# Kernel tuning notes

Hardware: AMD Instinct MI355X
Metric: run time of the kernel (lower is better)

Reference implementation:

```python
import jax, jax.numpy as jnp
from jax import lax
import numpy as np

BETA, TAU, NUM_ITER = 0.33, 1.0, 5
DN = ('NCDHW', 'OIDHW', 'NCDHW')


def _base_kernels():
    # 3x3x3 neighborhood-counting kernels from the torch module
    K_N6 = np.zeros((3, 3, 3), np.float32)
    for c in [(1, 1, 0), (1, 1, 2), (1, 0, 1), (1, 2, 1), (0, 1, 1), (2, 1, 1)]:
        K_N6[c] = 1.0
    K_N26 = np.ones((3, 3, 3), np.float32); K_N26[1, 1, 1] = 0.0
    K_N18 = K_N26.copy()
    for c in [(0, 0, 0), (0, 0, 2), (0, 2, 0), (0, 2, 2), (2, 0, 0), (2, 0, 2), (2, 2, 0), (2, 2, 2)]:
        K_N18[c] = 0.0
    K_B26 = np.zeros((3, 3, 3), np.float32)
    K_B26[0, 0, 0] = 1.0
    for c in [(0, 0, 1), (0, 1, 0), (0, 1, 1), (1, 0, 0), (1, 0, 1), (1, 1, 0)]:
        K_B26[c] = -1.0
    K_A6 = np.zeros((3, 3, 3), np.float32)
    K_A6[0, 1, 1] = -1.0
    for c in [(0, 0, 1), (0, 1, 0), (0, 1, 2), (0, 2, 1)]:
        K_A6[c] = 1.0
    return K_N6, K_N26, K_N18, K_B26, K_A6


def _stacked_weight():
    # Fuse all 17 simple-check convolutions into one conv over a 3-channel input
    # channel 0: img, channel 1: 1-img, channel 2: 2*img-1
    K_N6, K_N26, K_N18, K_B26, K_A6 = _base_kernels()
    b26 = [K_B26] + [np.flip(K_B26, ax) for ax in [(0,), (1,), (2,), (0, 1), (0, 2), (1, 2), (0, 1, 2)]]
    fA = np.flip(K_A6, 0)
    a6 = [K_A6, np.rot90(K_A6, axes=(0, 1)), np.rot90(K_A6, axes=(0, 2)),
          fA, np.rot90(fA, axes=(0, 1)), np.rot90(fA, axes=(0, 2))]
    rows = []
    def put(k, ch):
        w = np.zeros((3, 3, 3, 3), np.float32)
        w[ch] = k
        rows.append(w)
    put(K_N6, 1)   # counts bg 6-neighbors (applied to 1-img)
    put(K_N26, 0)  # counts fg 26-neighbors
    put(K_N18, 0)  # counts fg 18-neighbors
    for k in b26:
        put(k, 2)  # 8 B26-cell detectors on 2*img-1
    for k in a6:
        put(k, 2)  # 6 A6-cell detectors on 2*img-1
    return jnp.asarray(np.stack(rows)), jnp.asarray(K_N26).reshape(1, 1, 3, 3, 3)


W_SIMPLE, W_N26 = _stacked_weight()


def _clip01(x):  # F.hardtanh(x, 0, 1)
    return jnp.clip(x, 0.0, 1.0)


def _endpoint_check(img):
    p = jnp.pad(img, ((0, 0), (0, 0), (1, 1), (1, 1), (1, 1)))
    n26 = lax.conv_general_dilated(p, W_N26, (1, 1, 1), 'VALID', dimension_numbers=DN)
    return _clip01(2.0 - n26)  # endpoint iff <=1 fg 26-neighbor


def _simple_check(img):
    p = jnp.pad(img, ((0, 0), (0, 0), (1, 1), (1, 1), (1, 1)))
    x3 = jnp.concatenate([p, 1.0 - p, 2.0 * p - 1.0], axis=1)
    f = lax.conv_general_dilated(x3, W_SIMPLE, (2, 2, 2), 'VALID', dimension_numbers=DN)
    n6, n26, n18 = f[:, 0:1], f[:, 1:2], f[:, 2:3]
    num_b26 = jax.nn.relu(f[:, 3:11] - 6.0).sum(axis=1, keepdims=True)
    num_a6 = jax.nn.relu(f[:, 11:17] - 4.0).sum(axis=1, keepdims=True)
    cond1 = _clip01(n6) * _clip01(2.0 - n6)                              # exactly one bg 6-neighbor
    cond2 = _clip01(n26) * _clip01(2.0 - n26)                            # exactly one fg 26-neighbor
    cond3 = _clip01(n18) * _clip01(2.0 - n18) * _clip01(1.0 - num_b26)   # one 18-neighbor, no B26 cell
    cond4 = _clip01(n6 - 1.0) * _clip01(1.0 - num_a6) * _clip01(1.0 - num_b26)  # >=2 bg 6-nb, no A6/B26 cell
    return _clip01(cond1 + cond2 + cond3 + cond4)


def _forward(img):
    # _prepare_input: zero-pad each spatial dim by 1
    img = jnp.pad(img, ((0, 0), (0, 0), (1, 1), (1, 1), (1, 1)))
    # _stochastic_discretization (reparametrization + straight-through)
    alpha = (img + 1e-8) / (1.0 - img + 1e-8)
    u = jax.random.uniform(jax.random.key(42), img.shape, img.dtype, 1e-8, 1.0 - 1e-8)
    noise = jnp.log(u) - jnp.log1p(-u)
    soft = jax.nn.sigmoid((jnp.log(alpha) + noise * BETA) / TAU)
    img = lax.stop_gradient((soft > 0.5).astype(soft.dtype) - soft) + soft
    offsets = [(0, 0, 0), (1, 0, 0), (0, 1, 0), (1, 1, 0), (0, 0, 1), (1, 0, 1), (0, 1, 1), (1, 1, 1)]
    for _ in range(NUM_ITER):
        is_end = _endpoint_check(img)
        for xo, yo, zo in offsets:
            is_simple = _simple_check(img[:, :, xo:, yo:, zo:])
            sl = (slice(None), slice(None), slice(xo, None, 2), slice(yo, None, 2), slice(zo, None, 2))
            del_cand = is_simple * (1.0 - is_end[sl])
            img = img.at[sl].set(jnp.minimum(img[sl], 1.0 - del_cand))
    # _prepare_output: strip padding
    return img[:, :, 1:-1, 1:-1, 1:-1]


def setup_inputs():
    key = jax.random.key(0)
    img = jax.random.uniform(key, (2, 1, 160, 160, 160), jnp.float32)  # probabilities in [0,1)
    return {"img": img}


def reference(img):
    return _forward(img)
```

## Files before the change

kernel.cpp:

```cpp
#include <hip/hip_runtime.h>
#include <stdint.h>

#pragma clang fp contract(off)

#define PDIM 162
#define NW   (2*PDIM*PDIM*3)
#define NWH  (NW/2)
#define OD   160

#define PZ 97
#define LADDR(lz,ly) ((lz)*PZ + (ly)*3)

__device__ __forceinline__ uint32_t rotl32(uint32_t x, uint32_t r) {
  return (x << r) | (x >> (32u - r));
}

__device__ __forceinline__ uint32_t threefry_bits(uint32_t idx) {
  const uint32_t ks0 = 0u, ks1 = 42u, ks2 = 0x1BD11BDAu ^ 0u ^ 42u;
  uint32_t x0 = 0u + ks0;
  uint32_t x1 = idx + ks1;
#define TFR(r) { x0 += x1; x1 = rotl32(x1, (r)); x1 ^= x0; }
  TFR(13u) TFR(15u) TFR(26u) TFR(6u)
  x0 += ks1; x1 += ks2 + 1u;
  TFR(17u) TFR(29u) TFR(16u) TFR(24u)
  x0 += ks2; x1 += ks0 + 2u;
  TFR(13u) TFR(15u) TFR(26u) TFR(6u)
  x0 += ks0; x1 += ks1 + 3u;
  TFR(17u) TFR(29u) TFR(16u) TFR(24u)
  x0 += ks1; x1 += ks2 + 4u;
  TFR(13u) TFR(15u) TFR(26u) TFR(6u)
  x0 += ks2; x1 += ks0 + 5u;
#undef TFR
  return x0 ^ x1;
}

__device__ __forceinline__ float xla_logf(float xin) {
  uint32_t bits = __float_as_uint(xin);
  float e = (float)((int)(bits >> 23) - 126);
  float x = __uint_as_float((bits & 0x007fffffu) | 0x3f000000u);
  const float SQRTHF = 0.707106781186547524f;
  bool lt = (x < SQRTHF);
  float tmp = lt ? x : 0.0f;
  e = e - (lt ? 1.0f : 0.0f);
  x = x - 1.0f;
  x = x + tmp;
  float z = x * x;
  float y = 7.0376836292e-2f;
  y = fmaf(y, x, -1.1514610310e-1f);
  y = fmaf(y, x,  1.1676998740e-1f);
  y = fmaf(y, x, -1.2420140846e-1f);
  y = fmaf(y, x,  1.4249322787e-1f);
  y = fmaf(y, x, -1.6668057665e-1f);
  y = fmaf(y, x,  2.0000714765e-1f);
  y = fmaf(y, x, -2.4999993993e-1f);
  y = fmaf(y, x,  3.3333331174e-1f);
  y = y * x;
  y = y * z;
  y = fmaf(e, -2.12194440e-4f, y);
  y = fmaf(-0.5f, z, y);
  x = x + y;
  x = fmaf(e, 0.693359375f, x);
  return x;
}

__device__ __forceinline__ float xla_log1pf(float x) {
  float for_large = xla_logf(x + 1.0f);
  float for_small = fmaf(-0.5f, x, 1.0f) * x;
  return (fabsf(x) < 1e-4f) ? for_small : for_large;
}

__device__ __forceinline__ bool bin_pred(const float* __restrict__ in, uint32_t w,
                                         uint32_t lane) {
  uint32_t row = w / 3u, wx = w - row * 3u;
  uint32_t n  = row / (uint32_t)(PDIM * PDIM);
  uint32_t rr = row - n * (uint32_t)(PDIM * PDIM);
  uint32_t z  = rr / (uint32_t)PDIM;
  uint32_t y  = rr - z * (uint32_t)PDIM;
  uint32_t x  = wx * 64u + lane;
  if ((z - 1u) >= 160u || (y - 1u) >= 160u || (x - 1u) >= 160u) return false;
  float v = in[((n * 160u + (z - 1u)) * 160u + (y - 1u)) * 160u + (x - 1u)];
  uint32_t i = row * 162u + x;
  uint32_t b = threefry_bits(i);
  float f  = __uint_as_float((b >> 9) | 0x3f800000u) - 1.0f;
  float uu = fmaxf(1e-8f, f + 1e-8f);
  float h  = (v + 1e-8f) / ((1.0f - v) + 1e-8f);
  const float T = 1.1920928955078125e-7f;

  const float LN2 = 0.6931471805599453f;
  float la_f = __builtin_amdgcn_logf(h) * LN2;
  float nz_f = (__builtin_amdgcn_logf(uu) - __builtin_amdgcn_logf(1.0f - uu)) * LN2;
  float zs_f = fmaf(nz_f, 0.33f, la_f);
  if (fabsf(zs_f - T) > 3.0e-4f) return zs_f > T;

  float la = xla_logf(h);
  float noise = xla_logf(uu) - xla_log1pf(-uu);
  float zs = la + noise * 0.33f;
  return zs > T;
}

__global__ __launch_bounds__(256) void k_binarize(const float* __restrict__ in,
                                                  uint64_t* __restrict__ bits) {
  uint32_t t = blockIdx.x * 256u + threadIdx.x;
  uint32_t w0 = t >> 6, lane = t & 63u;
  if (w0 >= (uint32_t)NWH) return;
  uint32_t w1 = w0 + (uint32_t)NWH;
  bool p0 = bin_pred(in, w0, lane);
  bool p1 = bin_pred(in, w1, lane);
  uint64_t m0 = __ballot(p0);
  uint64_t m1 = __ballot(p1);
  if (lane == 0) { bits[w0] = m0; bits[w1] = m1; }
}

#define NB(dz,dy,dx) ((dx)==-1 ? Lb[(dz)+1][(dy)+1] : ((dx)==1 ? Rb[(dz)+1][(dy)+1] : Vv[(dz)+1][(dy)+1]))

#define GATHER_W(SRC, lz, ly, w) \
  _Pragma("unroll") \
  for (int dz = 0; dz < 3; ++dz) \
    _Pragma("unroll") \
    for (int dy = 0; dy < 3; ++dy) { \
      int rb = LADDR((lz) + dz - 1, (ly) + dy - 1); \
      uint64_t r0 = SRC[rb], r1 = SRC[rb + 1], r2 = SRC[rb + 2]; \
      uint64_t b = ((w) == 0) ? r0 : (((w) == 1) ? r1 : r2); \
      uint64_t a = ((w) == 0) ? 0ull : (((w) == 1) ? r0 : r1); \
      uint64_t d = ((w) == 0) ? r1 : (((w) == 1) ? r2 : 0ull); \
      Vv[dz][dy] = b; \
      Lb[dz][dy] = (b << 1) | (a >> 63); \
      Rb[dz][dy] = (b >> 1) | (d << 63); \
    }

struct OG { uint64_t o, g; };
__device__ __forceinline__ OG og_leaf2(uint64_t a, uint64_t b) {
  OG r; r.o = a | b; r.g = a & b; return r;
}
__device__ __forceinline__ OG og_comb(OG a, OG b) {
  OG r; r.g = a.g | b.g | (a.o & b.o); r.o = a.o | b.o; return r;
}

#define OG_BUILD_18_C(og18, ogc) \
  OG a0 = og_leaf2(NB(-1,0,0), NB(1,0,0)); \
  OG a1 = og_leaf2(NB(0,-1,0), NB(0,1,0)); \
  OG a2 = og_leaf2(NB(0,0,-1), NB(0,0,1)); \
  OG e0 = og_leaf2(NB(-1,-1,0), NB(-1,1,0)); \
  OG e1 = og_leaf2(NB(-1,0,-1), NB(-1,0,1)); \
  OG e2 = og_leaf2(NB(1,-1,0),  NB(1,1,0)); \
  OG e3 = og_leaf2(NB(1,0,-1),  NB(1,0,1)); \
  OG e4 = og_leaf2(NB(0,-1,-1), NB(0,-1,1)); \
  OG e5 = og_leaf2(NB(0,1,-1),  NB(0,1,1)); \
  OG t0 = og_comb(a0, a1); \
  OG t1 = og_comb(a2, e0); \
  OG t2 = og_comb(e1, e2); \
  OG t3 = og_comb(e3, e4); \
  OG og18 = og_comb(og_comb(og_comb(t0, t1), og_comb(t2, t3)), e5); \
  OG c0 = og_leaf2(NB(-1,-1,-1), NB(-1,-1,1)); \
  OG c1 = og_leaf2(NB(-1,1,-1),  NB(-1,1,1)); \
  OG c2 = og_leaf2(NB(1,-1,-1),  NB(1,-1,1)); \
  OG c3 = og_leaf2(NB(1,1,-1),   NB(1,1,1)); \
  OG ogc = og_comb(og_comb(c0, c1), og_comb(c2, c3));

__global__ __launch_bounds__(1024) void k_iter(const uint64_t* __restrict__ bin,
                                               uint64_t* __restrict__ bout,
                                               float4* __restrict__ outf,
                                               int zero_pads) {
  __shared__ uint64_t Bt[32 * PZ];
  __shared__ uint64_t Ge[32 * PZ];
  const int tid = threadIdx.x;
  const int bid = blockIdx.x;
  const int n  = bid / 100;
  const int rm = bid - n * 100;
  const int tz = rm / 10, ty = rm - tz * 10;
  const int gz0 = 1 + 16 * tz, gy0 = 1 + 16 * ty;

  if (zero_pads && bid == 0) {
    for (int j = tid; j < 1288; j += 1024) {
      int nn, z, y;
      if (j < 648) { nn = j / 324; int r = j - nn * 324;
                     z = (r >= 162) ? 161 : 0; y = (r >= 162) ? r - 162 : r; }
      else { int j2 = j - 648; nn = j2 / 320; int r = j2 - nn * 320;
             y = (r >= 160) ? 161 : 0; z = 1 + ((r >= 160) ? r - 160 : r); }
      uint64_t* p = bout + (((nn * 162 + z) * 162) + y) * 3;
      p[0] = 0; p[1] = 0; p[2] = 0;
    }
  }

  for (int ti = tid; ti < 32 * 32 * 3; ti += 1024) {
    int w = ti % 3, r = ti / 3, ly = r % 32, lz = r / 32;
    int z = gz0 - 8 + lz, y = gy0 - 8 + ly;
    uint64_t v = 0;
    if ((unsigned)z < 162u && (unsigned)y < 162u)
      v = bin[((n * 162 + z) * 162 + y) * 3 + w];
    Bt[LADDR(lz, ly) + w] = v;
  }
  __syncthreads();

  for (int ti = tid; ti < 30 * 30 * 3; ti += 1024) {
    int w = ti % 3, r = ti / 3, iy = r % 30, iz = r / 30;
    int lz = 1 + iz, ly = 1 + iy;
    int base = LADDR(lz, ly) + w;
    uint64_t res = 0;
    if (Bt[base] != 0ull) {
      uint64_t Vv[3][3], Lb[3][3], Rb[3][3];
      GATHER_W(Bt, lz, ly, w)
      OG_BUILD_18_C(og18, ogc)
      res = og_comb(og18, ogc).g;
    }
    Ge[base] = res;
  }
  __syncthreads();

  const int PLZ[8] = {1,0,1,0,1,0,1,0};
  const int PLY[8] = {1,1,0,0,1,1,0,0};
#pragma unroll
  for (int k = 0; k < 8; ++k) {
    const int h = 7 - k, cnt1 = 8 + h;
    const uint64_t xmask = (k < 4) ? 0x5555555555555555ull : 0xAAAAAAAAAAAAAAAAull;
    const int s0 = 8 - h;
    const int slz = s0 + ((s0 ^ PLZ[k]) & 1);
    const int sly = s0 + ((s0 ^ PLY[k]) & 1);
    for (int ti = tid; ti < cnt1 * cnt1 * 3; ti += 1024) {
      int w = ti % 3, r = ti / 3, iy = r % cnt1, iz = r / cnt1;
      int lz = slz + 2 * iz, ly = sly + 2 * iy;
      int base = LADDR(lz, ly) + w;
      uint64_t center = Bt[base];
      uint64_t act = center & xmask & Ge[base];
      if (act == 0ull) continue;
      uint64_t Vv[3][3], Lb[3][3], Rb[3][3];
      GATHER_W(Bt, lz, ly, w)

      OG_BUILD_18_C(og18, ogc)
      OG og26 = og_comb(og18, ogc);
      uint64_t e18 = og18.o & ~og18.g;
      uint64_t e26 = og26.o & ~og26.g;

      uint64_t m0f = ~NB(-1,0,0), m1f = ~NB(1,0,0), m2f = ~NB(0,-1,0);
      uint64_t m3f = ~NB(0,1,0),  m4f = ~NB(0,0,-1), m5f = ~NB(0,0,1);
      OG p0 = og_leaf2(m0f, m1f);
      OG p1 = og_leaf2(m2f, m3f);
      OG p2 = og_leaf2(m4f, m5f);
      OG pm = og_comb(og_comb(p0, p1), p2);
      uint64_t c6eq5 = pm.o & ~pm.g;
      uint64_t c6le4 = pm.g;

      uint64_t del = (c6eq5 | e26) & act;
      uint64_t need = act & ~del & (e18 | c6le4);
      if (need != 0ull) {
        uint64_t badB = 0;
#pragma unroll
        for (int sz = -1; sz <= 1; sz += 2)
#pragma unroll
          for (int sy = -1; sy <= 1; sy += 2)
#pragma unroll
            for (int sx = -1; sx <= 1; sx += 2) {
              uint64_t oct = NB(sz,0,0) | NB(0,sy,0) | NB(0,0,sx)
                           | NB(sz,sy,0) | NB(sz,0,sx) | NB(0,sy,sx);
              badB |= NB(sz,sy,sx) & ~oct;
            }
        uint64_t b0ok = ~badB;

        uint64_t badA = 0;
        badA |= ~NB(-1,0,0) & NB(-1,-1,0) & NB(-1,1,0) & NB(-1,0,-1) & NB(-1,0,1);
        badA |= ~NB( 1,0,0) & NB( 1,-1,0) & NB( 1,1,0) & NB( 1,0,-1) & NB( 1,0,1);
        badA |= ~NB(0,-1,0) & NB(-1,-1,0) & NB(1,-1,0) & NB(0,-1,-1) & NB(0,-1,1);
        badA |= ~NB(0, 1,0) & NB(-1, 1,0) & NB(1, 1,0) & NB(0, 1,-1) & NB(0, 1,1);
        badA |= ~NB(0,0,-1) & NB(-1,0,-1) & NB(1,0,-1) & NB(0,-1,-1) & NB(0,1,-1);
        badA |= ~NB(0,0, 1) & NB(-1,0, 1) & NB(1,0, 1) & NB(0,-1, 1) & NB(0,1, 1);
        uint64_t a0ok = ~badA;

        del |= ((e18 & b0ok) | (c6le4 & a0ok & b0ok)) & act;
      }
      if (del) Bt[base] = center & ~del;
    }
    __syncthreads();
  }

  if (outf) {
    for (int ti = tid; ti < 16 * 16 * 40; ti += 1024) {
      int g = ti % 40, r = ti / 40, iy = r % 16, iz = r / 16;
      int base = LADDR(8 + iz, 8 + iy);
      int bi = 1 + 4 * g;
      int wx = bi >> 6, sft = bi & 63;
      uint64_t v = Bt[base + wx] >> sft;
      if (sft > 60) v |= Bt[base + wx + 1] << (64 - sft);
      outf[((n * 160 + (gz0 + iz - 1)) * 160 + (gy0 + iy - 1)) * 40 + g] =
          make_float4((float)(v & 1u), (float)((v >> 1) & 1u),
                      (float)((v >> 2) & 1u), (float)((v >> 3) & 1u));
    }
  } else {
    for (int ti = tid; ti < 16 * 16 * 3; ti += 1024) {
      int w = ti % 3, r = ti / 3, iy = r % 16, iz = r / 16;
      bout[((n * 162 + gz0 + iz) * 162 + (gy0 + iy)) * 3 + w] =
          Bt[LADDR(8 + iz, 8 + iy) + w];
    }
  }
}

extern "C" void kernel_launch(void* const* d_in, const int* in_sizes, int n_in,
                              void* d_out, int out_size, void* d_ws, size_t ws_size,
                              hipStream_t stream) {
  const float* in = (const float*)d_in[0];
  float4* out = (float4*)d_out;
  uint64_t* A = (uint64_t*)d_ws;
  uint64_t* B = A + NW;

  k_binarize<<<dim3((NWH * 64 + 255) / 256), dim3(256), 0, stream>>>(in, A);
  k_iter<<<dim3(200), dim3(1024), 0, stream>>>(A, B, nullptr, 1);
  k_iter<<<dim3(200), dim3(1024), 0, stream>>>(B, A, nullptr, 0);
  k_iter<<<dim3(200), dim3(1024), 0, stream>>>(A, B, nullptr, 0);
  k_iter<<<dim3(200), dim3(1024), 0, stream>>>(B, A, nullptr, 0);
  k_iter<<<dim3(200), dim3(1024), 0, stream>>>(A, nullptr, out, 0);
}
```

Measured before the change: 213.2 us.

## Precompute neighbor-count mask in a separate kernel instead of per-tile halo recompute

Moves the per-iteration 'at least 2 fg 26-neighbors' mask computation out of the tiled iteration kernel into a standalone wide-grid kernel that writes a global mask buffer. The iteration kernel then loads the mask for its 30x30 region from global memory instead of recomputing it over a redundant halo with only 200 blocks. This removes halo recomputation and spreads the work across many more threads, at the cost of five extra launches and an additional global buffer round-trip. It also needs extra workspace for the mask buffer.

```diff
diff --git a/kernel.cpp b/kernel.cpp
--- a/kernel.cpp
+++ b/kernel.cpp
@@ -157,12 +157,42 @@
   OG c3 = og_leaf2(NB(1,1,-1),   NB(1,1,1)); \
   OG ogc = og_comb(og_comb(c0, c1), og_comb(c2, c3));
 
+__global__ __launch_bounds__(256) void k_ge2(const uint64_t* __restrict__ board,
+                                             uint64_t* __restrict__ Ge) {
+  int ti = blockIdx.x * 256 + threadIdx.x;
+  int w = ti % 3;  int r = ti / 3;
+  int y = 1 + (r % 160);  int rr = r / 160;
+  int z = 1 + (rr % 160); int n = rr / 160;
+  int idx = ((n * 162 + z) * 162 + y) * 3 + w;
+  uint64_t res = 0;
+  if (board[idx] != 0ull) {
+    uint64_t Vv[3][3], Lb[3][3], Rb[3][3];
+#pragma unroll
+    for (int dz = 0; dz < 3; ++dz)
+#pragma unroll
+      for (int dy = 0; dy < 3; ++dy) {
+        const uint64_t* p = board + ((n * 162 + z - 1 + dz) * 162 + (y - 1 + dy)) * 3;
+        uint64_t r0 = p[0], r1 = p[1], r2 = p[2];
+        uint64_t b = (w == 0) ? r0 : ((w == 1) ? r1 : r2);
+        uint64_t a = (w == 0) ? 0ull : ((w == 1) ? r0 : r1);
+        uint64_t d = (w == 0) ? r1 : ((w == 1) ? r2 : 0ull);
+        Vv[dz][dy] = b;
+        Lb[dz][dy] = (b << 1) | (a >> 63);
+        Rb[dz][dy] = (b >> 1) | (d << 63);
+      }
+    OG_BUILD_18_C(og18, ogc)
+    res = og_comb(og18, ogc).g;
+  }
+  Ge[idx] = res;
+}
+
 __global__ __launch_bounds__(1024) void k_iter(const uint64_t* __restrict__ bin,
+                                               const uint64_t* __restrict__ gein,
                                                uint64_t* __restrict__ bout,
                                                float4* __restrict__ outf,
                                                int zero_pads) {
   __shared__ uint64_t Bt[32 * PZ];
-  __shared__ uint64_t Ge[32 * PZ];
+  __shared__ uint64_t Gl[32 * PZ];
   const int tid = threadIdx.x;
   const int bid = blockIdx.x;
   const int n  = bid / 100;
@@ -190,20 +220,13 @@
       v = bin[((n * 162 + z) * 162 + y) * 3 + w];
     Bt[LADDR(lz, ly) + w] = v;
   }
-  __syncthreads();
-
   for (int ti = tid; ti < 30 * 30 * 3; ti += 1024) {
     int w = ti % 3, r = ti / 3, iy = r % 30, iz = r / 30;
-    int lz = 1 + iz, ly = 1 + iy;
-    int base = LADDR(lz, ly) + w;
-    uint64_t res = 0;
-    if (Bt[base] != 0ull) {
-      uint64_t Vv[3][3], Lb[3][3], Rb[3][3];
-      GATHER_W(Bt, lz, ly, w)
-      OG_BUILD_18_C(og18, ogc)
-      res = og_comb(og18, ogc).g;
-    }
-    Ge[base] = res;
+    int z = gz0 - 7 + iz, y = gy0 - 7 + iy;
+    uint64_t v = 0;
+    if ((unsigned)(z - 1) < 160u && (unsigned)(y - 1) < 160u)
+      v = gein[((n * 162 + z) * 162 + y) * 3 + w];
+    Gl[LADDR(1 + iz, 1 + iy) + w] = v;
   }
   __syncthreads();
 
@@ -221,7 +244,7 @@
       int lz = slz + 2 * iz, ly = sly + 2 * iy;
       int base = LADDR(lz, ly) + w;
       uint64_t center = Bt[base];
-      uint64_t act = center & xmask & Ge[base];
+      uint64_t act = center & xmask & Gl[base];
       if (act == 0ull) continue;
       uint64_t Vv[3][3], Lb[3][3], Rb[3][3];
       GATHER_W(Bt, lz, ly, w)
@@ -300,11 +323,18 @@
   float4* out = (float4*)d_out;
   uint64_t* A = (uint64_t*)d_ws;
   uint64_t* B = A + NW;
+  uint64_t* G = B + NW;
 
   k_binarize<<<dim3((NWH * 64 + 255) / 256), dim3(256), 0, stream>>>(in, A);
-  k_iter<<<dim3(200), dim3(1024), 0, stream>>>(A, B, nullptr, 1);
-  k_iter<<<dim3(200), dim3(1024), 0, stream>>>(B, A, nullptr, 0);
-  k_iter<<<dim3(200), dim3(1024), 0, stream>>>(A, B, nullptr, 0);
-  k_iter<<<dim3(200), dim3(1024), 0, stream>>>(B, A, nullptr, 0);
-  k_iter<<<dim3(200), dim3(1024), 0, stream>>>(A, nullptr, out, 0);
-}
+
+  k_ge2<<<dim3(600), dim3(256), 0, stream>>>(A, G);
+  k_iter<<<dim3(200), dim3(1024), 0, stream>>>(A, G, B, nullptr, 1);
+  k_ge2<<<dim3(600), dim3(256), 0, stream>>>(B, G);
+  k_iter<<<dim3(200), dim3(1024), 0, stream>>>(B, G, A, nullptr, 0);
+  k_ge2<<<dim3(600), dim3(256), 0, stream>>>(A, G);
+  k_iter<<<dim3(200), dim3(1024), 0, stream>>>(A, G, B, nullptr, 0);
+  k_ge2<<<dim3(600), dim3(256), 0, stream>>>(B, G);
+  k_iter<<<dim3(200), dim3(1024), 0, stream>>>(B, G, A, nullptr, 0);
+  k_ge2<<<dim3(600), dim3(256), 0, stream>>>(A, G);
+  k_iter<<<dim3(200), dim3(1024), 0, stream>>>(A, G, nullptr, out, 0);
+}
```

Measured after the change: 216.7 us. About the same (+1.6%).
